# Kernel optimization log

Measured on AMD Instinct MI355X. Metric: run time of the kernel, lower is better.

The kernel has to match this reference:

```python
import jax, jax.numpy as jnp
import numpy as np


def setup_inputs() -> dict:
    key = jax.random.key(0)
    k_w, k_xi, k_u = jax.random.split(key, 3)
    N, d, M, L, B = 4096, 512, 256, 16, 1024
    W = 2 * L + 1  # window width = 33
    # xavier-normal-ish scale for weight (fan_in=d, fan_out=M*W per torch xavier on last dim pairs)
    w_scale = (2.0 / (W + d)) ** 0.5
    xi_scale = (2.0 / (M + N + 2 * L)) ** 0.5
    weight = jax.random.normal(k_w, (M, W, d), dtype=jnp.float32) * w_scale
    bias = jnp.zeros((M, W, 1), dtype=jnp.float32)
    xi = jax.random.normal(k_xi, (M, N + 2 * L), dtype=jnp.float32) * xi_scale
    u = jax.random.normal(k_u, (B, d), dtype=jnp.float32)
    return {"u": u, "weight": weight, "bias": bias, "xi": xi}


def reference(u, weight, bias, xi):
    # weight: [M, W, d], bias: [M, W, 1], xi: [M, N + W - 1], u: [B, d]
    M, W, d = weight.shape
    N = xi.shape[1] - (W - 1)
    # first_step: G[m, j, b] = sigmoid(sum_k weight[m,j,k] * u[b,k] + bias[m,j])
    G = jax.nn.sigmoid(jnp.einsum('mjd,bd->mjb', weight, u) + bias)  # [M, W, B]
    # im2col-style unfold of xi into overlapping windows, replacing the N-step Python loop
    idx = jnp.arange(N)[:, None] + jnp.arange(W)[None, :]  # [N, W]
    Xw = xi[:, idx]  # [M, N, W]
    # out[n, b] = sum_{m, j} xi[m, n+j] * G[m, j, b]  == torch.cat of iter_prod rows
    return jnp.einsum('mnj,mjb->nb', Xw, G)  # [N, B]
```

## Files before the change

### kernel.cpp

```cpp
#include <hip/hip_runtime.h>
#include <hip/hip_bf16.h>

typedef __attribute__((ext_vector_type(8))) short bf16x8;
typedef __attribute__((ext_vector_type(4))) float f32x4;
typedef unsigned int u32;
typedef unsigned short u16;

#define XI_ROW 4128
#define KP     8448
#define NB     1024
#define NN     4096
#define DDIM   512

__device__ __forceinline__ u16 f2bf(float f) {
  union { float f; unsigned u; } c; c.f = f;
  return (u16)((c.u + 0x7FFFu + ((c.u >> 16) & 1u)) >> 16);
}
__device__ __forceinline__ float bf2f(u16 h) {
  union { u32 u; float f; } c; c.u = ((u32)h) << 16; return c.f;
}
__device__ __forceinline__ u32 pk2bf(float a, float b) {
  return (u32)f2bf(a) | ((u32)f2bf(b) << 16);
}
__device__ __forceinline__ void gld16(const u16* g, u16* l) {
  __builtin_amdgcn_global_load_lds(
      (const __attribute__((address_space(1))) u32*)(const void*)g,
      (__attribute__((address_space(3))) u32*)(void*)l, 16, 0, 0);
}

#define BAR() __builtin_amdgcn_s_barrier()
#define LGKM0() asm volatile("s_waitcnt lgkmcnt(0)" ::: "memory")
#define WAITVM(N) asm volatile("s_waitcnt vmcnt(" #N ")" ::: "memory")
#define SCHED0() __builtin_amdgcn_sched_barrier(0)

__global__ __launch_bounds__(256) void k_prep(
    const float* __restrict__ w, const float* __restrict__ u,
    const float* __restrict__ xi, u16* __restrict__ Wbf,
    u16* __restrict__ Ubf, u16* __restrict__ xiT) {
  __shared__ u16 tile[32][33];
  const int bx = blockIdx.x, t = threadIdx.x;
  if (bx < 4224) {
    int kp = bx * 2 + (t >> 7), tl = t & 127;
    int m = kp & 255, j = kp >> 8;
    float4 v = ((const float4*)(w + (size_t)(m * 33 + j) * DDIM))[tl];
    ((uint2*)(Wbf + (size_t)kp * DDIM))[tl] =
        make_uint2(pk2bf(v.x, v.y), pk2bf(v.z, v.w));
  } else if (bx < 4736) {
    int b = (bx - 4224) * 2 + (t >> 7), tl = t & 127;
    float4 v = ((const float4*)(u + (size_t)b * DDIM))[tl];
    ((uint2*)(Ubf + (size_t)b * DDIM))[tl] =
        make_uint2(pk2bf(v.x, v.y), pk2bf(v.z, v.w));
  } else {
    int bx2 = bx - 4736;
    int cblk = bx2 % 129, mblk = bx2 / 129;
    int c0 = cblk * 32, m0 = mblk * 32;
    int tx = t & 31, ty = t >> 5;
#pragma unroll
    for (int i = 0; i < 4; ++i)
      tile[ty + i * 8][tx] = f2bf(xi[(size_t)(m0 + ty + i * 8) * XI_ROW + c0 + tx]);
    __syncthreads();
#pragma unroll
    for (int i = 0; i < 4; ++i)
      xiT[(size_t)(c0 + ty + i * 8) * 256 + m0 + tx] = tile[tx][ty + i * 8];
  }
}

template<int KSTEPS, int AS, int BS>
__device__ __forceinline__ void gemm_pipeline(
    const u16* __restrict__ aSrc, const u16* __restrict__ bSrc,
    u16* As0, u16* As1, u16* Bl0, u16* Bl1,
    int wid, int wr, int wc, int rl, int kg, int rl7,
    f32x4 (&acc)[4][4]) {

  auto stage = [&](u16* Ab, u16* Bb, int kk) {
#pragma unroll
    for (int i = 0; i < 4; ++i)
      gld16(aSrc + (size_t)i * 8 * AS + kk, &Ab[(wid * 4 + i) * 512]);
#pragma unroll
    for (int i = 0; i < 4; ++i)
      gld16(bSrc + (size_t)i * 8 * BS + kk, &Bb[(wid * 4 + i) * 512]);
  };
  auto compute = [&](const u16* Ab, const u16* Bb) {
#pragma unroll
    for (int kh = 0; kh < 2; ++kh) {
      bf16x8 af[4], bfv[4];
#pragma unroll
      for (int fm = 0; fm < 4; ++fm)
        af[fm] = *(const bf16x8*)&Ab[(wr * 64 + fm * 16 + rl) * 64 +
                                     (((kh * 4 + kg) ^ rl7) * 8)];
#pragma unroll
      for (int fn = 0; fn < 4; ++fn)
        bfv[fn] = *(const bf16x8*)&Bb[(wc * 64 + fn * 16 + rl) * 64 +
                                      (((kh * 4 + kg) ^ rl7) * 8)];
      __builtin_amdgcn_s_setprio(1);
#pragma unroll
      for (int fm = 0; fm < 4; ++fm)
#pragma unroll
        for (int fn = 0; fn < 4; ++fn)
          acc[fm][fn] = __builtin_amdgcn_mfma_f32_16x16x32_bf16(
              af[fm], bfv[fn], acc[fm][fn], 0, 0, 0);
      __builtin_amdgcn_s_setprio(0);
    }
  };

  stage(As0, Bl0, 0);
  WAITVM(0);
  BAR();
#pragma unroll 1
  for (int ts = 0; ts < KSTEPS - 2; ts += 2) {
    stage(As1, Bl1, (ts + 1) * 64);
    WAITVM(8);
    BAR();
    compute(As0, Bl0);
    BAR();
    stage(As0, Bl0, (ts + 2) * 64);
    WAITVM(8);
    BAR();
    compute(As1, Bl1);
    BAR();
  }
  stage(As1, Bl1, (KSTEPS - 1) * 64);
  WAITVM(8);
  BAR();
  compute(As0, Bl0);
  BAR();
  WAITVM(0);
  BAR();
  compute(As1, Bl1);
}

__global__ __launch_bounds__(256) void k_gemm1(
    const u16* __restrict__ Wbf, const u16* __restrict__ Ubf,
    const float* __restrict__ Bsrc, u16* __restrict__ Gt) {
  __shared__ u16 As0[8192], As1[8192], Bl0[8192], Bl1[8192];
  const int r0 = blockIdx.x * 128;
  const int b0 = blockIdx.y * 128;
  const int t = threadIdx.x, lane = t & 63, wid = t >> 6;
  const int wr = wid >> 1, wc = wid & 1;
  const int rl = lane & 15, kg = lane >> 4, rl7 = rl & 7;
  const int lr = lane >> 3, lc = (lane & 7) ^ (lr & 7);
  const u16* aSrc = Wbf + (size_t)(r0 + wid * 32 + lr) * DDIM + lc * 8;
  const u16* bSrc = Ubf + (size_t)(b0 + wid * 32 + lr) * DDIM + lc * 8;

  f32x4 acc[4][4] = {};
  gemm_pipeline<8, DDIM, DDIM>(aSrc, bSrc, As0, As1, Bl0, Bl1,
                               wid, wr, wc, rl, kg, rl7, acc);

#pragma unroll
  for (int fm = 0; fm < 4; ++fm) {
    int kbase = r0 + wr * 64 + fm * 16 + kg * 4;
    float b4[4];
#pragma unroll
    for (int r = 0; r < 4; ++r) {
      int kk = kbase + r;
      b4[r] = Bsrc[(kk & 255) * 33 + (kk >> 8)];
    }
#pragma unroll
    for (int fn = 0; fn < 4; ++fn) {
      int b = b0 + wc * 64 + fn * 16 + rl;
      u16 o[4];
#pragma unroll
      for (int r = 0; r < 4; ++r) {
        float x = acc[fm][fn][r] + b4[r];
        o[r] = f2bf(1.0f / (1.0f + __expf(-x)));
      }
      u16* dst = Gt + (size_t)b * KP + kbase;
      *(u32*)(dst)     = (u32)o[0] | ((u32)o[1] << 16);
      *(u32*)(dst + 2) = (u32)o[2] | ((u32)o[3] << 16);
    }
  }
}

__global__ __launch_bounds__(512, 2) void k_gemm2(
    const u16* __restrict__ xiT, const u16* __restrict__ Gt,
    float* __restrict__ Out, u16* __restrict__ Part) {
  __shared__ u16 lds[65536];
  const int lid = blockIdx.x;
  const int b0 = (lid & 3) * 256;
  const int ks = (lid >> 2) & 3;
  const int n0 = (lid >> 4) * 256;
  const int kOff = (ks < 2) ? ks * 2176 : 4352 + (ks - 2) * 2048;
  const int nt = (ks < 2) ? 34 : 32;

  const int t = threadIdx.x, lane = t & 63, wid = t >> 6;
  const int wr = wid >> 2, wc = wid & 3;
  const int rl = lane & 15, kg = lane >> 4, rl7 = rl & 7;
  const int sr = lane >> 3;
  const int sc = (lane & 7) ^ sr;

  const u16* aS = xiT + (size_t)(n0 + wid * 16 + sr) * 256 + kOff + sc * 8;
  const u16* bS = Gt  + (size_t)(b0 + wid * 16 + sr) * KP  + kOff + sc * 8;

  f32x4 acc[8][4] = {};
  bf16x8 af[8], b01[4], b23[4];

  auto stA = [&](int tile, int half, int buf) {
    u16* d = lds + (buf * 4 + half) * 8192 + wid * 1024;
    const u16* s = aS + (size_t)half * 32768 + (size_t)tile * 64;
    gld16(s, d);
    gld16(s + 2048, d + 512);
  };
  auto stB = [&](int tile, int half, int buf) {
    u16* d = lds + (buf * 4 + 2 + half) * 8192 + wid * 1024;
    const u16* s = bS + (size_t)half * 128 * KP + (size_t)tile * 64;
    gld16(s, d);
    gld16(s + (size_t)8 * KP, d + 512);
  };
  auto rdA = [&](int buf, int sub) {
    const u16* p = lds + (buf * 4 + wr) * 8192;
#pragma unroll
    for (int q = 0; q < 4; ++q)
#pragma unroll
      for (int kh = 0; kh < 2; ++kh)
        af[q * 2 + kh] = *(const bf16x8*)
            &p[((sub * 4 + q) * 16 + rl) * 64 + (((kh * 4 + kg) ^ rl7) * 8)];
  };
  auto rdB = [&](int buf, int sub, bf16x8 (&bq)[4]) {
    const u16* p = lds + (buf * 4 + 2 + (wc >> 1)) * 8192;
#pragma unroll
    for (int q = 0; q < 2; ++q)
#pragma unroll
      for (int kh = 0; kh < 2; ++kh)
        bq[q * 2 + kh] = *(const bf16x8*)
            &p[((wc & 1) * 64 + (sub * 2 + q) * 16 + rl) * 64 +
               (((kh * 4 + kg) ^ rl7) * 8)];
  };
  auto mm = [&](int sm, int sn, bf16x8 (&bq)[4]) {
    __builtin_amdgcn_s_setprio(1);
#pragma unroll
    for (int q = 0; q < 4; ++q)
#pragma unroll
      for (int p = 0; p < 2; ++p)
#pragma unroll
        for (int kh = 0; kh < 2; ++kh)
          acc[sm * 4 + q][sn * 2 + p] = __builtin_amdgcn_mfma_f32_16x16x32_bf16(
              af[q * 2 + kh], bq[p * 2 + kh], acc[sm * 4 + q][sn * 2 + p], 0, 0, 0);
    __builtin_amdgcn_s_setprio(0);
  };

  auto runIter = [&](int T, bool s2) {
    rdA(0, 0); rdB(0, 0, b01); stA(T + 1, 0, 1);
    SCHED0(); BAR(); LGKM0(); SCHED0(); mm(0, 0, b01); BAR();
    rdB(0, 1, b23); stA(T + 1, 1, 1);
    SCHED0(); BAR(); LGKM0(); SCHED0(); mm(0, 1, b23); BAR();
    rdA(0, 1); if (s2) stB(T + 2, 0, 0);
    SCHED0(); BAR(); LGKM0(); SCHED0(); mm(1, 0, b01); BAR();
    if (s2) { stB(T + 2, 1, 0); WAITVM(4); } else { WAITVM(0); }
    SCHED0(); BAR(); SCHED0(); mm(1, 1, b23); BAR();
    rdA(1, 0); rdB(1, 0, b01); if (s2) stA(T + 2, 0, 0);
    SCHED0(); BAR(); LGKM0(); SCHED0(); mm(0, 0, b01); BAR();
    rdB(1, 1, b23); if (s2) stA(T + 2, 1, 0);
    SCHED0(); BAR(); LGKM0(); SCHED0(); mm(0, 1, b23); BAR();
    rdA(1, 1); if (s2) stB(T + 3, 0, 1);
    SCHED0(); BAR(); LGKM0(); SCHED0(); mm(1, 0, b01); BAR();
    if (s2) { stB(T + 3, 1, 1); WAITVM(4); }
    SCHED0(); BAR(); SCHED0(); mm(1, 1, b23); BAR();
  };

  stA(0, 0, 0); stA(0, 1, 0); stB(0, 0, 0); stB(0, 1, 0);
  stB(1, 0, 1); stB(1, 1, 1);
  WAITVM(4);
  BAR();

  const int nIter = nt >> 1;
#pragma unroll 1
  for (int it = 0; it < nIter - 1; ++it) runIter(it * 2, true);
  runIter((nIter - 1) * 2, false);

  if (ks == 0) {
#pragma unroll
    for (int fm = 0; fm < 8; ++fm)
#pragma unroll
      for (int fn = 0; fn < 4; ++fn) {
        int n = n0 + wr * 128 + fm * 16 + kg * 4;
        int b = b0 + wc * 64 + fn * 16 + rl;
#pragma unroll
        for (int r = 0; r < 4; ++r)
          Out[(size_t)(n + r) * NB + b] = acc[fm][fn][r];
      }
  } else {
    u16* P = Part + (size_t)(ks - 1) * (NN * NB);
#pragma unroll
    for (int fm = 0; fm < 8; ++fm)
#pragma unroll
      for (int fn = 0; fn < 4; ++fn) {
        int n = n0 + wr * 128 + fm * 16 + kg * 4;
        int b = b0 + wc * 64 + fn * 16 + rl;
#pragma unroll
        for (int r = 0; r < 4; ++r)
          P[(size_t)(n + r) * NB + b] = f2bf(acc[fm][fn][r]);
      }
  }
}

__global__ __launch_bounds__(256) void k_reduce(float* __restrict__ Out,
                                                const u16* __restrict__ Part) {
  size_t i = (size_t)blockIdx.x * 256 + threadIdx.x;
  float4 a = ((const float4*)Out)[i];
#pragma unroll
  for (int p = 0; p < 3; ++p) {
    ushort4 v = ((const ushort4*)(Part + (size_t)p * (NN * NB)))[i];
    a.x += bf2f(v.x); a.y += bf2f(v.y); a.z += bf2f(v.z); a.w += bf2f(v.w);
  }
  ((float4*)Out)[i] = a;
}

extern "C" void kernel_launch(void* const* d_in, const int* in_sizes, int n_in,
                              void* d_out, int out_size, void* d_ws, size_t ws_size,
                              hipStream_t stream) {
  const float* u  = (const float*)d_in[0];
  const float* w  = (const float*)d_in[1];
  const float* bs = (const float*)d_in[2];
  const float* xi = (const float*)d_in[3];
  float* out = (float*)d_out;

  u16* xiT  = (u16*)d_ws;
  u16* Gt   = (u16*)((char*)d_ws + 2113536);
  u16* Wbf  = (u16*)((char*)d_ws + 19415040);
  u16* Ubf  = (u16*)((char*)d_ws + 28065792);
  u16* Part = (u16*)((char*)d_ws + 19415040);

  k_prep<<<5768, 256, 0, stream>>>(w, u, xi, Wbf, Ubf, xiT);
  k_gemm1<<<dim3(66, 8), 256, 0, stream>>>(Wbf, Ubf, bs, Gt);
  k_gemm2<<<256, 512, 0, stream>>>(xiT, Gt, out, Part);
  k_reduce<<<4096, 256, 0, stream>>>(out, Part);
}
```

Baseline: 107.1 us.

## Fuse split-K reduction into gemm2 using last-arriving-block atomic counter

Removes the separate k_reduce kernel. Each split-K block of gemm2 now increments a per-tile atomic counter after writing its partial, and the last of the four blocks for a tile sums the fp32 output and the bf16 partials, using its own registers for its own slice. The counters are zeroed by an extra block in k_prep. This saves a kernel launch and one full pass over the output, at the cost of a fence and serialized tail work in the last block of each tile.

Result: slower. 261.7 us (+144.3%).

```diff
diff --git a/kernel.cpp b/kernel.cpp
--- a/kernel.cpp
+++ b/kernel.cpp
@@ -27,6 +27,12 @@
       (const __attribute__((address_space(1))) u32*)(const void*)g,
       (__attribute__((address_space(3))) u32*)(void*)l, 16, 0, 0);
 }
+__device__ __forceinline__ float ldf32_agent(const float* p) {
+  return __hip_atomic_load(p, __ATOMIC_RELAXED, __HIP_MEMORY_SCOPE_AGENT);
+}
+__device__ __forceinline__ u32 ldu32_agent(const u32* p) {
+  return __hip_atomic_load(p, __ATOMIC_RELAXED, __HIP_MEMORY_SCOPE_AGENT);
+}
 
 #define BAR() __builtin_amdgcn_s_barrier()
 #define LGKM0() asm volatile("s_waitcnt lgkmcnt(0)" ::: "memory")
@@ -36,7 +42,8 @@
 __global__ __launch_bounds__(256) void k_prep(
     const float* __restrict__ w, const float* __restrict__ u,
     const float* __restrict__ xi, u16* __restrict__ Wbf,
-    u16* __restrict__ Ubf, u16* __restrict__ xiT) {
+    u16* __restrict__ Ubf, u16* __restrict__ xiT,
+    u32* __restrict__ cnt) {
   __shared__ u16 tile[32][33];
   const int bx = blockIdx.x, t = threadIdx.x;
   if (bx < 4224) {
@@ -50,7 +57,7 @@
     float4 v = ((const float4*)(u + (size_t)b * DDIM))[tl];
     ((uint2*)(Ubf + (size_t)b * DDIM))[tl] =
         make_uint2(pk2bf(v.x, v.y), pk2bf(v.z, v.w));
-  } else {
+  } else if (bx < 5768) {
     int bx2 = bx - 4736;
     int cblk = bx2 % 129, mblk = bx2 / 129;
     int c0 = cblk * 32, m0 = mblk * 32;
@@ -62,6 +69,8 @@
 #pragma unroll
     for (int i = 0; i < 4; ++i)
       xiT[(size_t)(c0 + ty + i * 8) * 256 + m0 + tx] = tile[tx][ty + i * 8];
+  } else {
+    if (t < 64) cnt[t] = 0;
   }
 }
 
@@ -173,7 +182,7 @@
 
 __global__ __launch_bounds__(512, 2) void k_gemm2(
     const u16* __restrict__ xiT, const u16* __restrict__ Gt,
-    float* __restrict__ Out, u16* __restrict__ Part) {
+    float* __restrict__ Out, u16* __restrict__ Part, u32* __restrict__ cnt) {
   __shared__ u16 lds[65536];
   const int lid = blockIdx.x;
   const int b0 = (lid & 3) * 256;
@@ -291,18 +300,42 @@
           P[(size_t)(n + r) * NB + b] = f2bf(acc[fm][fn][r]);
       }
   }
-}
-
-__global__ __launch_bounds__(256) void k_reduce(float* __restrict__ Out,
-                                                const u16* __restrict__ Part) {
-  size_t i = (size_t)blockIdx.x * 256 + threadIdx.x;
-  float4 a = ((const float4*)Out)[i];
-#pragma unroll
-  for (int p = 0; p < 3; ++p) {
-    ushort4 v = ((const ushort4*)(Part + (size_t)p * (NN * NB)))[i];
-    a.x += bf2f(v.x); a.y += bf2f(v.y); a.z += bf2f(v.z); a.w += bf2f(v.w);
-  }
-  ((float4*)Out)[i] = a;
+
+  __threadfence();
+  __syncthreads();
+  u32* flagp = (u32*)lds;
+  if (t == 0) *flagp = atomicAdd(&cnt[(lid >> 4) * 4 + (lid & 3)], 1u);
+  __syncthreads();
+  if (*flagp == 3) {
+    __threadfence();
+    const u32* P32[3] = {
+        (const u32*)Part, (const u32*)(Part + (size_t)(NN * NB)),
+        (const u32*)(Part + (size_t)2 * (NN * NB))};
+#pragma unroll
+    for (int fm = 0; fm < 8; ++fm)
+#pragma unroll
+      for (int fn = 0; fn < 4; ++fn) {
+        int n = n0 + wr * 128 + fm * 16 + kg * 4;
+        int b = b0 + wc * 64 + fn * 16 + rl;
+#pragma unroll
+        for (int r = 0; r < 4; ++r) {
+          size_t a = (size_t)(n + r) * NB + b;
+          float s = (ks == 0) ? acc[fm][fn][r] : ldf32_agent(&Out[a]);
+#pragma unroll
+          for (int c = 0; c < 3; ++c) {
+            float v;
+            if (ks == c + 1) {
+              v = bf2f(f2bf(acc[fm][fn][r]));
+            } else {
+              u32 wv = ldu32_agent(&P32[c][a >> 1]);
+              v = bf2f((u16)((a & 1) ? (wv >> 16) : (wv & 0xFFFFu)));
+            }
+            s += v;
+          }
+          Out[a] = s;
+        }
+      }
+  }
 }
 
 extern "C" void kernel_launch(void* const* d_in, const int* in_sizes, int n_in,
@@ -319,9 +352,9 @@
   u16* Wbf  = (u16*)((char*)d_ws + 19415040);
   u16* Ubf  = (u16*)((char*)d_ws + 28065792);
   u16* Part = (u16*)((char*)d_ws + 19415040);
-
-  k_prep<<<5768, 256, 0, stream>>>(w, u, xi, Wbf, Ubf, xiT);
+  u32* cnt  = (u32*)((char*)d_ws + 44580864);
+
+  k_prep<<<5769, 256, 0, stream>>>(w, u, xi, Wbf, Ubf, xiT, cnt);
   k_gemm1<<<dim3(66, 8), 256, 0, stream>>>(Wbf, Ubf, bs, Gt);
-  k_gemm2<<<256, 512, 0, stream>>>(xiT, Gt, out, Part);
-  k_reduce<<<4096, 256, 0, stream>>>(out, Part);
-}
+  k_gemm2<<<256, 512, 0, stream>>>(xiT, Gt, out, Part, cnt);
+}
```
